# Optimization experiments

Hardware: AMD Instinct MI355X
Metric: run time of the kernel (lower is better)

The kernel has to match this reference:

```python
import jax, jax.numpy as jnp
import numpy as np

N, DEG, F_IN, H = 50000, 16, 128, 32
E = N * DEG


def _linear_params(key, out_f, in_f):
    kw, kb = jax.random.split(key)
    s = 1.0 / np.sqrt(in_f)
    W = jax.random.uniform(kw, (out_f, in_f), jnp.float32, -s, s)
    b = jax.random.uniform(kb, (out_f,), jnp.float32, -s, s)
    return W, b


def setup_inputs() -> dict:
    key = jax.random.key(0)
    ks = jax.random.split(key, 12)
    X = jax.random.normal(ks[0], (N, F_IN), jnp.float32)
    # DEG distinct nonzero offsets shared by all rows -> unique (src,dst) pairs,
    # so the COO tensor is already coalesced (no duplicate indices).
    offsets = jax.random.permutation(ks[1], jnp.arange(1, N))[:DEG]
    src = jnp.repeat(jnp.arange(N, dtype=jnp.int32), DEG)
    dst = ((src.reshape(N, DEG) + offsets[None, :].astype(jnp.int32)) % N).reshape(-1)
    D = jax.ops.segment_sum(jnp.ones((E,), jnp.float32), src, num_segments=N)
    wn1p, bn1p = _linear_params(ks[2], H, F_IN)      # convN1.pass_map
    wn1s, bn1s = _linear_params(ks[3], H, F_IN)      # convN1.self_map
    we1p, be1p = _linear_params(ks[4], H, 2 * H)     # convE1.pass_map
    we1s, be1s = _linear_params(ks[5], H, F_IN)      # convE1.self_map
    wn2p, bn2p = _linear_params(ks[6], H, H)         # convN2.pass_map
    wn2s, bn2s = _linear_params(ks[7], H, H)         # convN2.self_map
    we2p, be2p = _linear_params(ks[8], H, 2 * H)     # convE2.pass_map
    we2s, be2s = _linear_params(ks[9], H, H)         # convE2.self_map
    wc, bc = _linear_params(ks[10], 1, H)            # classifier
    return dict(X=X, src=src, dst=dst, D=D,
                wn1p=wn1p, bn1p=bn1p, wn1s=wn1s, bn1s=bn1s,
                we1p=we1p, be1p=be1p, we1s=we1s, be1s=be1s,
                wn2p=wn2p, bn2p=bn2p, wn2s=wn2s, bn2s=bn2s,
                we2p=we2p, be2p=be2p, we2s=we2s, be2s=be2s,
                wc=wc, bc=bc)


def reference(X, src, dst, D,
              wn1p, bn1p, wn1s, bn1s,
              we1p, be1p, we1s, be1s,
              wn2p, bn2p, wn2s, bn2s,
              we2p, be2p, we2s, be2s,
              wc, bc):
    n = X.shape[0]

    def node_conv(vals, Xn, wp, bp, ws, bs):
        # torch.sparse.sum(A, dim=1): sum edge values per source row
        Asum = jax.ops.segment_sum(vals, src, num_segments=n)
        return jax.nn.relu((Asum / D[:, None]) @ wp.T + bp + Xn @ ws.T + bs)

    def edge_conv(vals, Xn, wp, bp, ws, bs):
        X1, X2 = Xn[src], Xn[dst]
        Ef = jnp.concatenate([(X1 - X2) * 0.5, (X1 + X2) * 0.5], axis=-1)
        return jax.nn.relu(Ef @ wp.T + bp + vals @ ws.T + bs)

    # add_graph: edge features = |X[src] - X[dst]|
    vals0 = jnp.abs(X[src] - X[dst])            # (E, F_IN)
    X0 = jnp.zeros_like(X)                       # forward zeros node features
    Xn1 = node_conv(vals0, X0, wn1p, bn1p, wn1s, bn1s)   # (N, 32)
    vals1 = edge_conv(vals0, Xn1, we1p, be1p, we1s, be1s)  # (E, 32)
    Xn2 = node_conv(vals1, Xn1, wn2p, bn2p, wn2s, bn2s)  # (N, 32)
    vals2 = edge_conv(vals1, Xn2, we2p, be2p, we2s, be2s)  # (E, 32)
    SX = jax.nn.sigmoid(vals2 @ wc.T + bc)[:, 0]          # (E,)
    return SX
```

## Files before the change

### kernel.cpp

```cpp
#include <hip/hip_runtime.h>

#define DEG 16
#define F_IN 128
#define H 32

typedef __attribute__((ext_vector_type(8))) _Float16 f16x8;
typedef __attribute__((ext_vector_type(4))) float f32x4;
typedef __attribute__((ext_vector_type(4))) int i32x4;

union HS  { _Float16 f; unsigned short s; };
union HF4 { _Float16 h[4]; uint2 u; };

__device__ __forceinline__ float relu_f(float x) { return fmaxf(x, 0.0f); }

__device__ __forceinline__ f16x8 habs8(f16x8 a) {
    union { f16x8 h; i32x4 i; } u; u.h = a;
#pragma unroll
    for (int k = 0; k < 4; ++k) u.i[k] &= 0x7FFF7FFF;
    return u.h;
}

__global__ __launch_bounds__(256) void k_xhalf(
    const float* __restrict__ X, _Float16* __restrict__ Xh, long n8)
{
    const long t = (long)blockIdx.x * 256 + threadIdx.x;
    if (t >= n8) return;
    const float4* p = (const float4*)X + t * 2;
    const float4 a = p[0], b = p[1];
    f16x8 h;
    h[0] = (_Float16)a.x; h[1] = (_Float16)a.y; h[2] = (_Float16)a.z; h[3] = (_Float16)a.w;
    h[4] = (_Float16)b.x; h[5] = (_Float16)b.y; h[6] = (_Float16)b.z; h[7] = (_Float16)b.w;
    *(f16x8*)(Xh + t * 8) = h;
}

__global__ __launch_bounds__(256) void k_prep(
    const float* __restrict__ we1s, const float* __restrict__ we1p,
    const float* __restrict__ be1p, const float* __restrict__ be1s,
    const float* __restrict__ we2p, const float* __restrict__ we2s,
    const float* __restrict__ be2p, const float* __restrict__ be2s,
    const float* __restrict__ wn1p, const float* __restrict__ bn1p,
    const float* __restrict__ bn1s,
    const float* __restrict__ wn2p, const float* __restrict__ bn2p,
    const float* __restrict__ wn2s, const float* __restrict__ bn2s,
    _Float16* __restrict__ Wcat1, _Float16* __restrict__ Wcat2,
    _Float16* __restrict__ Wn1ph,
    _Float16* __restrict__ Wn2ph, _Float16* __restrict__ Wn2sh,
    float* __restrict__ bias1, float* __restrict__ bias2,
    float* __restrict__ biasn1, float* __restrict__ biasn2)
{
    const int t0 = blockIdx.x * 256 + threadIdx.x;
    const int stride = gridDim.x * 256;
    for (int idx = t0; idx < 32 * 192; idx += stride) {
        const int n = idx / 192, k = idx - n * 192;
        float w;
        if (k < 128)       w = we1s[n * 128 + k];
        else if (k < 160)  w = 0.5f * we1p[n * 64 + (k - 128)];
        else               w = 0.5f * we1p[n * 64 + 32 + (k - 160)];
        Wcat1[idx] = (_Float16)w;
    }
    for (int idx = t0; idx < 32 * 96; idx += stride) {
        const int n = idx / 96, k = idx - n * 96;
        float w;
        if (k < 32)       w = 0.5f * we2p[n * 64 + k];
        else if (k < 64)  w = 0.5f * we2p[n * 64 + 32 + (k - 32)];
        else              w = we2s[n * 32 + (k - 64)];
        Wcat2[idx] = (_Float16)w;
    }
    for (int idx = t0; idx < 32 * 128; idx += stride)
        Wn1ph[idx] = (_Float16)wn1p[idx];
    for (int idx = t0; idx < 32 * 32; idx += stride) {
        Wn2ph[idx] = (_Float16)wn2p[idx];
        Wn2sh[idx] = (_Float16)wn2s[idx];
    }
    if (t0 < H) {
        bias1[t0]  = be1p[t0] + be1s[t0];
        bias2[t0]  = be2p[t0] + be2s[t0];
        biasn1[t0] = bn1p[t0] + bn1s[t0];
        biasn2[t0] = bn2p[t0] + bn2s[t0];
    }
}

__global__ __launch_bounds__(64, 3) void k_p1(
    const _Float16* __restrict__ Xh, const int* __restrict__ dst,
    const float* __restrict__ D,
    const _Float16* __restrict__ Wcat1, const _Float16* __restrict__ Wn1ph,
    const float* __restrict__ biasn1,
    _Float16* __restrict__ t1h, _Float16* __restrict__ Xn1h, int N)
{
    const int lane = threadIdx.x;
    const int m = lane & 15, g = lane >> 4;
    const int i0 = blockIdx.x * 16;
    const int srow = (i0 + m < N) ? (i0 + m) : (N - 1);

    i32x4 dj4[4];
    {
        const i32x4* dp = (const i32x4*)(dst + (size_t)srow * DEG);
#pragma unroll
        for (int q = 0; q < 4; ++q) dj4[q] = dp[q];
    }
    f16x8 sv[4];
#pragma unroll
    for (int kb = 0; kb < 4; ++kb)
        sv[kb] = *(const f16x8*)(Xh + (size_t)srow * F_IN + kb * 32 + g * 8);
    f16x8 Bs[4][2], Bn[4][2];
#pragma unroll
    for (int kb = 0; kb < 4; ++kb)
#pragma unroll
        for (int t = 0; t < 2; ++t) {
            Bs[kb][t] = *(const f16x8*)(Wcat1 + (t * 16 + m) * 192 + kb * 32 + g * 8);
            Bn[kb][t] = *(const f16x8*)(Wn1ph + (t * 16 + m) * 128 + kb * 32 + g * 8);
        }

    f16x8 tvc[4], tvn[4];
#pragma unroll
    for (int kb = 0; kb < 4; ++kb)
        tvc[kb] = *(const f16x8*)(Xh + (size_t)dj4[0][0] * F_IN + kb * 32 + g * 8);

    f32x4 cn0 = {0.f,0.f,0.f,0.f}, cn1 = {0.f,0.f,0.f,0.f};
#pragma unroll
    for (int j = 0; j < 16; ++j) {
        if (j < 15) {
            const int dn = dj4[(j + 1) >> 2][(j + 1) & 3];
#pragma unroll
            for (int kb = 0; kb < 4; ++kb)
                tvn[kb] = *(const f16x8*)(Xh + (size_t)dn * F_IN + kb * 32 + g * 8);
        }
        f32x4 cs0 = {0.f,0.f,0.f,0.f}, cs1 = {0.f,0.f,0.f,0.f};
#pragma unroll
        for (int kb = 0; kb < 4; ++kb) {
            const f16x8 a = habs8(sv[kb] - tvc[kb]);
            cs0 = __builtin_amdgcn_mfma_f32_16x16x32_f16(a, Bs[kb][0], cs0, 0, 0, 0);
            cs1 = __builtin_amdgcn_mfma_f32_16x16x32_f16(a, Bs[kb][1], cs1, 0, 0, 0);
            cn0 = __builtin_amdgcn_mfma_f32_16x16x32_f16(a, Bn[kb][0], cn0, 0, 0, 0);
            cn1 = __builtin_amdgcn_mfma_f32_16x16x32_f16(a, Bn[kb][1], cn1, 0, 0, 0);
        }
        const size_t tb = ((size_t)blockIdx.x * 16 + j) * 512;
        HF4 a;
#pragma unroll
        for (int r = 0; r < 4; ++r) a.h[r] = (_Float16)cs0[r];
        *(uint2*)(t1h + tb + lane * 4) = a.u;
#pragma unroll
        for (int r = 0; r < 4; ++r) a.h[r] = (_Float16)cs1[r];
        *(uint2*)(t1h + tb + 256 + lane * 4) = a.u;
#pragma unroll
        for (int kb = 0; kb < 4; ++kb) tvc[kb] = tvn[kb];
    }
    const float bn0 = biasn1[m], bn1v = biasn1[16 + m];
#pragma unroll
    for (int r = 0; r < 4; ++r) {
        const int node = i0 + g * 4 + r;
        if (node < N) {
            const float invD = 1.0f / D[node];
            Xn1h[(size_t)node * H + m]      = (_Float16)relu_f(cn0[r] * invD + bn0);
            Xn1h[(size_t)node * H + 16 + m] = (_Float16)relu_f(cn1[r] * invD + bn1v);
        }
    }
}

__global__ __launch_bounds__(64, 4) void k_p2(
    const int* __restrict__ dst, const _Float16* __restrict__ Xn1h,
    const _Float16* __restrict__ Wcat1, const float* __restrict__ bias1,
    const _Float16* __restrict__ Wn2ph, const _Float16* __restrict__ Wn2sh,
    const float* __restrict__ biasn2, const float* __restrict__ D,
    _Float16* t1v1,
    _Float16* __restrict__ Xn2h, int N)
{
    __shared__ unsigned short RP[16 * 40];
    const int lane = threadIdx.x;
    const int m = lane & 15, g = lane >> 4;
    const int i0 = blockIdx.x * 16;
    const int srow = (i0 + m < N) ? (i0 + m) : (N - 1);

    i32x4 dj4[4];
    {
        const i32x4* dp = (const i32x4*)(dst + (size_t)srow * DEG);
#pragma unroll
        for (int q = 0; q < 4; ++q) dj4[q] = dp[q];
    }
    const f16x8 x1 = *(const f16x8*)(Xn1h + (size_t)srow * H + g * 8);
    f16x8 Bf[2][2];
#pragma unroll
    for (int kb = 0; kb < 2; ++kb)
#pragma unroll
        for (int t = 0; t < 2; ++t)
            Bf[kb][t] = *(const f16x8*)(Wcat1 + (t * 16 + m) * 192 + (4 + kb) * 32 + g * 8);

    f16x8 x2c, x2n;
    uint2 u0c, u1c, u0n, u1n;
    {
        const int d0 = dj4[0][0];
        x2c = *(const f16x8*)(Xn1h + (size_t)d0 * H + g * 8);
        const size_t tb = ((size_t)blockIdx.x * 16) * 512;
        u0c = *(const uint2*)(t1v1 + tb + lane * 4);
        u1c = *(const uint2*)(t1v1 + tb + 256 + lane * 4);
    }
    const float b0 = bias1[m], b1v = bias1[16 + m];
    f32x4 sB0 = {0.f,0.f,0.f,0.f}, sB1 = {0.f,0.f,0.f,0.f};
    const int rr = lane >> 2, qq = lane & 3;
#pragma unroll
    for (int j = 0; j < 16; ++j) {
        if (j < 15) {
            const int dn = dj4[(j + 1) >> 2][(j + 1) & 3];
            x2n = *(const f16x8*)(Xn1h + (size_t)dn * H + g * 8);
            const size_t tbn = ((size_t)blockIdx.x * 16 + j + 1) * 512;
            u0n = *(const uint2*)(t1v1 + tbn + lane * 4);
            u1n = *(const uint2*)(t1v1 + tbn + 256 + lane * 4);
        }
        f32x4 c0, c1;
        { HF4 a; a.u = u0c;
#pragma unroll
          for (int r = 0; r < 4; ++r) c0[r] = (float)a.h[r];
          a.u = u1c;
#pragma unroll
          for (int r = 0; r < 4; ++r) c1[r] = (float)a.h[r]; }
        const f16x8 ad = x1 - x2c;
        const f16x8 aS = x1 + x2c;
        c0 = __builtin_amdgcn_mfma_f32_16x16x32_f16(ad, Bf[0][0], c0, 0, 0, 0);
        c1 = __builtin_amdgcn_mfma_f32_16x16x32_f16(ad, Bf[0][1], c1, 0, 0, 0);
        c0 = __builtin_amdgcn_mfma_f32_16x16x32_f16(aS, Bf[1][0], c0, 0, 0, 0);
        c1 = __builtin_amdgcn_mfma_f32_16x16x32_f16(aS, Bf[1][1], c1, 0, 0, 0);
#pragma unroll
        for (int r = 0; r < 4; ++r) {
            const float v0 = relu_f(c0[r] + b0);
            const float v1 = relu_f(c1[r] + b1v);
            HS h0, h1; h0.f = (_Float16)v0; h1.f = (_Float16)v1;
            RP[(g * 4 + r) * 40 + m]      = h0.s;
            RP[(g * 4 + r) * 40 + 16 + m] = h1.s;
            sB0[r] += v0; sB1[r] += v1;
        }
        const size_t tb = ((size_t)blockIdx.x * 16 + j) * 512;
        const i32x4 v = *(const i32x4*)(RP + rr * 40 + qq * 8);
        *(i32x4*)(t1v1 + tb + rr * 32 + qq * 8) = v;
        x2c = x2n; u0c = u0n; u1c = u1n;
    }
    _Float16* RPh = (_Float16*)RP;
#pragma unroll
    for (int r = 0; r < 4; ++r) {
        const int node = i0 + g * 4 + r;
        const float invD = 1.0f / D[(node < N) ? node : (N - 1)];
        RPh[(g * 4 + r) * 40 + m]      = (_Float16)(sB0[r] * invD);
        RPh[(g * 4 + r) * 40 + 16 + m] = (_Float16)(sB1[r] * invD);
    }
    const f16x8 aF = *(const f16x8*)(RPh + m * 40 + g * 8);
    f16x8 Bp[2], Bs2[2];
#pragma unroll
    for (int t = 0; t < 2; ++t) {
        Bp[t]  = *(const f16x8*)(Wn2ph + (t * 16 + m) * H + g * 8);
        Bs2[t] = *(const f16x8*)(Wn2sh + (t * 16 + m) * H + g * 8);
    }
    f32x4 c0 = {0.f,0.f,0.f,0.f}, c1 = {0.f,0.f,0.f,0.f};
    c0 = __builtin_amdgcn_mfma_f32_16x16x32_f16(aF, Bp[0], c0, 0, 0, 0);
    c1 = __builtin_amdgcn_mfma_f32_16x16x32_f16(aF, Bp[1], c1, 0, 0, 0);
    c0 = __builtin_amdgcn_mfma_f32_16x16x32_f16(x1, Bs2[0], c0, 0, 0, 0);
    c1 = __builtin_amdgcn_mfma_f32_16x16x32_f16(x1, Bs2[1], c1, 0, 0, 0);
    const float bp0 = biasn2[m], bp1 = biasn2[16 + m];
#pragma unroll
    for (int r = 0; r < 4; ++r) {
        const int node = i0 + g * 4 + r;
        if (node < N) {
            Xn2h[(size_t)node * H + m]      = (_Float16)relu_f(c0[r] + bp0);
            Xn2h[(size_t)node * H + 16 + m] = (_Float16)relu_f(c1[r] + bp1);
        }
    }
}

__global__ __launch_bounds__(64, 4) void k_p3(
    const _Float16* __restrict__ Xn2h, const int* __restrict__ dst,
    const _Float16* __restrict__ vals1,
    const _Float16* __restrict__ Wcat2, const float* __restrict__ bias2,
    const float* __restrict__ wc, const float* __restrict__ bc,
    float* __restrict__ out, int N)
{
    __shared__ float outS[16 * 16];
    const int lane = threadIdx.x;
    const int m = lane & 15, g = lane >> 4;
    const int i0 = blockIdx.x * 16;
    const int srow = (i0 + m < N) ? (i0 + m) : (N - 1);

    i32x4 dj4[4];
    {
        const i32x4* dp = (const i32x4*)(dst + (size_t)srow * DEG);
#pragma unroll
        for (int q = 0; q < 4; ++q) dj4[q] = dp[q];
    }
    const f16x8 x1 = *(const f16x8*)(Xn2h + (size_t)srow * H + g * 8);
    f16x8 Bf[3][2];
#pragma unroll
    for (int kb = 0; kb < 3; ++kb)
#pragma unroll
        for (int t = 0; t < 2; ++t)
            Bf[kb][t] = *(const f16x8*)(Wcat2 + (t * 16 + m) * 96 + kb * 32 + g * 8);

    f16x8 x2b[2], avb[2];
#pragma unroll
    for (int s = 0; s < 2; ++s) {
        const int dn = dj4[s >> 2][s & 3];
        x2b[s] = *(const f16x8*)(Xn2h + (size_t)dn * H + g * 8);
        avb[s] = *(const f16x8*)(vals1 + ((size_t)blockIdx.x * 16 + s) * 512 + m * 32 + g * 8);
    }
    const float b0 = bias2[m], b1v = bias2[16 + m];
    const float w0 = wc[m], w1 = wc[16 + m];
#pragma unroll
    for (int j = 0; j < 16; ++j) {
        const int s = j & 1;
        const f16x8 x2 = x2b[s];
        const f16x8 av = avb[s];
        if (j < 14) {
            const int dn = dj4[(j + 2) >> 2][(j + 2) & 3];
            x2b[s] = *(const f16x8*)(Xn2h + (size_t)dn * H + g * 8);
            avb[s] = *(const f16x8*)(vals1 + ((size_t)blockIdx.x * 16 + j + 2) * 512 + m * 32 + g * 8);
        }
        const f16x8 ad = x1 - x2;
        const f16x8 aS = x1 + x2;
        f32x4 c0 = {0.f,0.f,0.f,0.f}, c1 = {0.f,0.f,0.f,0.f};
        c0 = __builtin_amdgcn_mfma_f32_16x16x32_f16(ad, Bf[0][0], c0, 0, 0, 0);
        c1 = __builtin_amdgcn_mfma_f32_16x16x32_f16(ad, Bf[0][1], c1, 0, 0, 0);
        c0 = __builtin_amdgcn_mfma_f32_16x16x32_f16(aS, Bf[1][0], c0, 0, 0, 0);
        c1 = __builtin_amdgcn_mfma_f32_16x16x32_f16(aS, Bf[1][1], c1, 0, 0, 0);
        c0 = __builtin_amdgcn_mfma_f32_16x16x32_f16(av, Bf[2][0], c0, 0, 0, 0);
        c1 = __builtin_amdgcn_mfma_f32_16x16x32_f16(av, Bf[2][1], c1, 0, 0, 0);

        float sr[4];
#pragma unroll
        for (int r = 0; r < 4; ++r)
            sr[r] = relu_f(c0[r] + b0) * w0 + relu_f(c1[r] + b1v) * w1;
#pragma unroll
        for (int mask = 1; mask < 16; mask <<= 1) {
#pragma unroll
            for (int r = 0; r < 4; ++r)
                sr[r] += __shfl_xor(sr[r], mask);
        }
        if (m == 0) {
#pragma unroll
            for (int r = 0; r < 4; ++r)
                outS[(g * 4 + r) * 16 + j] = sr[r];
        }
    }
    {
        const float bcv = bc[0];
        const float* s = outS + lane * 4;
        float4 o;
        o.x = 1.0f / (1.0f + __expf(-(s[0] + bcv)));
        o.y = 1.0f / (1.0f + __expf(-(s[1] + bcv)));
        o.z = 1.0f / (1.0f + __expf(-(s[2] + bcv)));
        o.w = 1.0f / (1.0f + __expf(-(s[3] + bcv)));
        if (i0 + 16 <= N || (i0 + (lane >> 2)) < N)
            *(float4*)(out + (size_t)i0 * DEG + lane * 4) = o;
    }
}

extern "C" void kernel_launch(void* const* d_in, const int* in_sizes, int n_in,
                              void* d_out, int out_size, void* d_ws, size_t ws_size,
                              hipStream_t stream)
{
    const float* X    = (const float*)d_in[0];
    const int*   dst  = (const int*)  d_in[2];
    const float* D    = (const float*)d_in[3];
    const float* wn1p = (const float*)d_in[4];
    const float* bn1p = (const float*)d_in[5];
    const float* bn1s = (const float*)d_in[7];
    const float* we1p = (const float*)d_in[8];
    const float* be1p = (const float*)d_in[9];
    const float* we1s = (const float*)d_in[10];
    const float* be1s = (const float*)d_in[11];
    const float* wn2p = (const float*)d_in[12];
    const float* bn2p = (const float*)d_in[13];
    const float* wn2s = (const float*)d_in[14];
    const float* bn2s = (const float*)d_in[15];
    const float* we2p = (const float*)d_in[16];
    const float* be2p = (const float*)d_in[17];
    const float* we2s = (const float*)d_in[18];
    const float* be2s = (const float*)d_in[19];
    const float* wc   = (const float*)d_in[20];
    const float* bc   = (const float*)d_in[21];

    const int N = in_sizes[3];
    const int nbW = (N + 15) / 16;
    const size_t Epad = (size_t)nbW * 16 * DEG;

    char* w = (char*)d_ws;
    _Float16* t1v1  = (_Float16*)w;  w += Epad * H * 2;
    _Float16* Xh    = (_Float16*)w;  w += (size_t)N * F_IN * 2;
    _Float16* Xn1h  = (_Float16*)w;  w += (size_t)N * H * 2;
    _Float16* Xn2h  = (_Float16*)w;  w += (size_t)N * H * 2;
    _Float16* Wcat1 = (_Float16*)w;  w += 32 * 192 * 2;
    _Float16* Wcat2 = (_Float16*)w;  w += 32 * 96 * 2;
    _Float16* Wn1ph = (_Float16*)w;  w += 32 * 128 * 2;
    _Float16* Wn2ph = (_Float16*)w;  w += 32 * 32 * 2;
    _Float16* Wn2sh = (_Float16*)w;  w += 32 * 32 * 2;
    float* bias1  = (float*)w;       w += H * 4;
    float* bias2  = (float*)w;       w += H * 4;
    float* biasn1 = (float*)w;       w += H * 4;
    float* biasn2 = (float*)w;       w += H * 4;
    float* outp = (float*)d_out;

    const long n8 = (long)N * F_IN / 8;
    const int nbX = (int)((n8 + 255) / 256);

    k_xhalf<<<nbX, 256, 0, stream>>>(X, Xh, n8);
    k_prep<<<32, 256, 0, stream>>>(we1s, we1p, be1p, be1s, we2p, we2s, be2p, be2s,
                                   wn1p, bn1p, bn1s, wn2p, bn2p, wn2s, bn2s,
                                   Wcat1, Wcat2, Wn1ph, Wn2ph, Wn2sh,
                                   bias1, bias2, biasn1, biasn2);
    k_p1<<<nbW, 64, 0, stream>>>(Xh, dst, D, Wcat1, Wn1ph, biasn1, t1v1, Xn1h, N);
    k_p2<<<nbW, 64, 0, stream>>>(dst, Xn1h, Wcat1, bias1, Wn2ph, Wn2sh,
                                 biasn2, D, t1v1, Xn2h, N);
    k_p3<<<nbW, 64, 0, stream>>>(Xn2h, dst, t1v1, Wcat2, bias2, wc, bc, outp, N);
}
```

Baseline: 199.7 us.

## Pack four waves per block and deepen gather prefetch to two edges

Each kernel now runs four independent 16-node chunks per 256-thread block instead of one wave per block, with per-wave shared-memory slices and early exit for out-of-range chunks. k_p1 and k_p2 switch from single-edge to two-edge-ahead double-buffered prefetch of the gathered neighbour rows. k_p1's MFMA loop is written out by hand. The aim is lower block-launch and scheduling overhead from tiny 64-thread blocks, plus more latency hiding for the random gathers. In exchange, register pressure rises under the new launch bounds, which could lower occupancy or cause spills.

```diff
diff --git a/kernel.cpp b/kernel.cpp
--- a/kernel.cpp
+++ b/kernel.cpp
@@ -80,16 +80,19 @@
     }
 }
 
-__global__ __launch_bounds__(64, 3) void k_p1(
+__global__ __launch_bounds__(256, 4) void k_p1(
     const _Float16* __restrict__ Xh, const int* __restrict__ dst,
     const float* __restrict__ D,
     const _Float16* __restrict__ Wcat1, const _Float16* __restrict__ Wn1ph,
     const float* __restrict__ biasn1,
     _Float16* __restrict__ t1h, _Float16* __restrict__ Xn1h, int N)
 {
-    const int lane = threadIdx.x;
+    const int wave = threadIdx.x >> 6;
+    const int lane = threadIdx.x & 63;
+    const int chunk = blockIdx.x * 4 + wave;
+    const int i0 = chunk * 16;
+    if (i0 >= N) return;
     const int m = lane & 15, g = lane >> 4;
-    const int i0 = blockIdx.x * 16;
     const int srow = (i0 + m < N) ? (i0 + m) : (N - 1);
 
     i32x4 dj4[4];
@@ -111,30 +114,46 @@
             Bn[kb][t] = *(const f16x8*)(Wn1ph + (t * 16 + m) * 128 + kb * 32 + g * 8);
         }
 
-    f16x8 tvc[4], tvn[4];
-#pragma unroll
-    for (int kb = 0; kb < 4; ++kb)
-        tvc[kb] = *(const f16x8*)(Xh + (size_t)dj4[0][0] * F_IN + kb * 32 + g * 8);
+    f16x8 tv[2][4];
+#pragma unroll
+    for (int s = 0; s < 2; ++s) {
+        const int dn = dj4[s >> 2][s & 3];
+#pragma unroll
+        for (int kb = 0; kb < 4; ++kb)
+            tv[s][kb] = *(const f16x8*)(Xh + (size_t)dn * F_IN + kb * 32 + g * 8);
+    }
 
     f32x4 cn0 = {0.f,0.f,0.f,0.f}, cn1 = {0.f,0.f,0.f,0.f};
 #pragma unroll
     for (int j = 0; j < 16; ++j) {
-        if (j < 15) {
-            const int dn = dj4[(j + 1) >> 2][(j + 1) & 3];
+        const int s = j & 1;
+        f16x8 a0 = tv[s][0], a1 = tv[s][1], a2 = tv[s][2], a3 = tv[s][3];
+        if (j < 14) {
+            const int dn = dj4[(j + 2) >> 2][(j + 2) & 3];
 #pragma unroll
             for (int kb = 0; kb < 4; ++kb)
-                tvn[kb] = *(const f16x8*)(Xh + (size_t)dn * F_IN + kb * 32 + g * 8);
-        }
+                tv[s][kb] = *(const f16x8*)(Xh + (size_t)dn * F_IN + kb * 32 + g * 8);
+        }
+        a0 = habs8(sv[0] - a0); a1 = habs8(sv[1] - a1);
+        a2 = habs8(sv[2] - a2); a3 = habs8(sv[3] - a3);
         f32x4 cs0 = {0.f,0.f,0.f,0.f}, cs1 = {0.f,0.f,0.f,0.f};
-#pragma unroll
-        for (int kb = 0; kb < 4; ++kb) {
-            const f16x8 a = habs8(sv[kb] - tvc[kb]);
-            cs0 = __builtin_amdgcn_mfma_f32_16x16x32_f16(a, Bs[kb][0], cs0, 0, 0, 0);
-            cs1 = __builtin_amdgcn_mfma_f32_16x16x32_f16(a, Bs[kb][1], cs1, 0, 0, 0);
-            cn0 = __builtin_amdgcn_mfma_f32_16x16x32_f16(a, Bn[kb][0], cn0, 0, 0, 0);
-            cn1 = __builtin_amdgcn_mfma_f32_16x16x32_f16(a, Bn[kb][1], cn1, 0, 0, 0);
-        }
-        const size_t tb = ((size_t)blockIdx.x * 16 + j) * 512;
+        cs0 = __builtin_amdgcn_mfma_f32_16x16x32_f16(a0, Bs[0][0], cs0, 0, 0, 0);
+        cs1 = __builtin_amdgcn_mfma_f32_16x16x32_f16(a0, Bs[0][1], cs1, 0, 0, 0);
+        cn0 = __builtin_amdgcn_mfma_f32_16x16x32_f16(a0, Bn[0][0], cn0, 0, 0, 0);
+        cn1 = __builtin_amdgcn_mfma_f32_16x16x32_f16(a0, Bn[0][1], cn1, 0, 0, 0);
+        cs0 = __builtin_amdgcn_mfma_f32_16x16x32_f16(a1, Bs[1][0], cs0, 0, 0, 0);
+        cs1 = __builtin_amdgcn_mfma_f32_16x16x32_f16(a1, Bs[1][1], cs1, 0, 0, 0);
+        cn0 = __builtin_amdgcn_mfma_f32_16x16x32_f16(a1, Bn[1][0], cn0, 0, 0, 0);
+        cn1 = __builtin_amdgcn_mfma_f32_16x16x32_f16(a1, Bn[1][1], cn1, 0, 0, 0);
+        cs0 = __builtin_amdgcn_mfma_f32_16x16x32_f16(a2, Bs[2][0], cs0, 0, 0, 0);
+        cs1 = __builtin_amdgcn_mfma_f32_16x16x32_f16(a2, Bs[2][1], cs1, 0, 0, 0);
+        cn0 = __builtin_amdgcn_mfma_f32_16x16x32_f16(a2, Bn[2][0], cn0, 0, 0, 0);
+        cn1 = __builtin_amdgcn_mfma_f32_16x16x32_f16(a2, Bn[2][1], cn1, 0, 0, 0);
+        cs0 = __builtin_amdgcn_mfma_f32_16x16x32_f16(a3, Bs[3][0], cs0, 0, 0, 0);
+        cs1 = __builtin_amdgcn_mfma_f32_16x16x32_f16(a3, Bs[3][1], cs1, 0, 0, 0);
+        cn0 = __builtin_amdgcn_mfma_f32_16x16x32_f16(a3, Bn[3][0], cn0, 0, 0, 0);
+        cn1 = __builtin_amdgcn_mfma_f32_16x16x32_f16(a3, Bn[3][1], cn1, 0, 0, 0);
+        const size_t tb = ((size_t)chunk * 16 + j) * 512;
         HF4 a;
 #pragma unroll
         for (int r = 0; r < 4; ++r) a.h[r] = (_Float16)cs0[r];
@@ -142,8 +161,6 @@
 #pragma unroll
         for (int r = 0; r < 4; ++r) a.h[r] = (_Float16)cs1[r];
         *(uint2*)(t1h + tb + 256 + lane * 4) = a.u;
-#pragma unroll
-        for (int kb = 0; kb < 4; ++kb) tvc[kb] = tvn[kb];
     }
     const float bn0 = biasn1[m], bn1v = biasn1[16 + m];
 #pragma unroll
@@ -157,7 +174,7 @@
     }
 }
 
-__global__ __launch_bounds__(64, 4) void k_p2(
+__global__ __launch_bounds__(256, 4) void k_p2(
     const int* __restrict__ dst, const _Float16* __restrict__ Xn1h,
     const _Float16* __restrict__ Wcat1, const float* __restrict__ bias1,
     const _Float16* __restrict__ Wn2ph, const _Float16* __restrict__ Wn2sh,
@@ -165,10 +182,14 @@
     _Float16* t1v1,
     _Float16* __restrict__ Xn2h, int N)
 {
-    __shared__ unsigned short RP[16 * 40];
-    const int lane = threadIdx.x;
+    __shared__ unsigned short RPall[4][16 * 40];
+    const int wave = threadIdx.x >> 6;
+    const int lane = threadIdx.x & 63;
+    const int chunk = blockIdx.x * 4 + wave;
+    const int i0 = chunk * 16;
+    if (i0 >= N) return;
+    unsigned short* RP = RPall[wave];
     const int m = lane & 15, g = lane >> 4;
-    const int i0 = blockIdx.x * 16;
     const int srow = (i0 + m < N) ? (i0 + m) : (N - 1);
 
     i32x4 dj4[4];
@@ -185,36 +206,40 @@
         for (int t = 0; t < 2; ++t)
             Bf[kb][t] = *(const f16x8*)(Wcat1 + (t * 16 + m) * 192 + (4 + kb) * 32 + g * 8);
 
-    f16x8 x2c, x2n;
-    uint2 u0c, u1c, u0n, u1n;
-    {
-        const int d0 = dj4[0][0];
-        x2c = *(const f16x8*)(Xn1h + (size_t)d0 * H + g * 8);
-        const size_t tb = ((size_t)blockIdx.x * 16) * 512;
-        u0c = *(const uint2*)(t1v1 + tb + lane * 4);
-        u1c = *(const uint2*)(t1v1 + tb + 256 + lane * 4);
+    f16x8 x2b[2];
+    uint2 u0b[2], u1b[2];
+#pragma unroll
+    for (int s = 0; s < 2; ++s) {
+        const int dn = dj4[s >> 2][s & 3];
+        x2b[s] = *(const f16x8*)(Xn1h + (size_t)dn * H + g * 8);
+        const size_t tb = ((size_t)chunk * 16 + s) * 512;
+        u0b[s] = *(const uint2*)(t1v1 + tb + lane * 4);
+        u1b[s] = *(const uint2*)(t1v1 + tb + 256 + lane * 4);
     }
     const float b0 = bias1[m], b1v = bias1[16 + m];
     f32x4 sB0 = {0.f,0.f,0.f,0.f}, sB1 = {0.f,0.f,0.f,0.f};
     const int rr = lane >> 2, qq = lane & 3;
 #pragma unroll
     for (int j = 0; j < 16; ++j) {
-        if (j < 15) {
-            const int dn = dj4[(j + 1) >> 2][(j + 1) & 3];
-            x2n = *(const f16x8*)(Xn1h + (size_t)dn * H + g * 8);
-            const size_t tbn = ((size_t)blockIdx.x * 16 + j + 1) * 512;
-            u0n = *(const uint2*)(t1v1 + tbn + lane * 4);
-            u1n = *(const uint2*)(t1v1 + tbn + 256 + lane * 4);
+        const int s = j & 1;
+        const f16x8 x2 = x2b[s];
+        const uint2 u0 = u0b[s], u1 = u1b[s];
+        if (j < 14) {
+            const int dn = dj4[(j + 2) >> 2][(j + 2) & 3];
+            x2b[s] = *(const f16x8*)(Xn1h + (size_t)dn * H + g * 8);
+            const size_t tbn = ((size_t)chunk * 16 + j + 2) * 512;
+            u0b[s] = *(const uint2*)(t1v1 + tbn + lane * 4);
+            u1b[s] = *(const uint2*)(t1v1 + tbn + 256 + lane * 4);
         }
         f32x4 c0, c1;
-        { HF4 a; a.u = u0c;
+        { HF4 a; a.u = u0;
 #pragma unroll
           for (int r = 0; r < 4; ++r) c0[r] = (float)a.h[r];
-          a.u = u1c;
+          a.u = u1;
 #pragma unroll
           for (int r = 0; r < 4; ++r) c1[r] = (float)a.h[r]; }
-        const f16x8 ad = x1 - x2c;
-        const f16x8 aS = x1 + x2c;
+        const f16x8 ad = x1 - x2;
+        const f16x8 aS = x1 + x2;
         c0 = __builtin_amdgcn_mfma_f32_16x16x32_f16(ad, Bf[0][0], c0, 0, 0, 0);
         c1 = __builtin_amdgcn_mfma_f32_16x16x32_f16(ad, Bf[0][1], c1, 0, 0, 0);
         c0 = __builtin_amdgcn_mfma_f32_16x16x32_f16(aS, Bf[1][0], c0, 0, 0, 0);
@@ -228,10 +253,9 @@
             RP[(g * 4 + r) * 40 + 16 + m] = h1.s;
             sB0[r] += v0; sB1[r] += v1;
         }
-        const size_t tb = ((size_t)blockIdx.x * 16 + j) * 512;
+        const size_t tb = ((size_t)chunk * 16 + j) * 512;
         const i32x4 v = *(const i32x4*)(RP + rr * 40 + qq * 8);
         *(i32x4*)(t1v1 + tb + rr * 32 + qq * 8) = v;
-        x2c = x2n; u0c = u0n; u1c = u1n;
     }
     _Float16* RPh = (_Float16*)RP;
 #pragma unroll
@@ -264,17 +288,21 @@
     }
 }
 
-__global__ __launch_bounds__(64, 4) void k_p3(
+__global__ __launch_bounds__(256, 4) void k_p3(
     const _Float16* __restrict__ Xn2h, const int* __restrict__ dst,
     const _Float16* __restrict__ vals1,
     const _Float16* __restrict__ Wcat2, const float* __restrict__ bias2,
     const float* __restrict__ wc, const float* __restrict__ bc,
     float* __restrict__ out, int N)
 {
-    __shared__ float outS[16 * 16];
-    const int lane = threadIdx.x;
+    __shared__ float outSall[4][16 * 16];
+    const int wave = threadIdx.x >> 6;
+    const int lane = threadIdx.x & 63;
+    const int chunk = blockIdx.x * 4 + wave;
+    const int i0 = chunk * 16;
+    if (i0 >= N) return;
+    float* outS = outSall[wave];
     const int m = lane & 15, g = lane >> 4;
-    const int i0 = blockIdx.x * 16;
     const int srow = (i0 + m < N) ? (i0 + m) : (N - 1);
 
     i32x4 dj4[4];
@@ -296,7 +324,7 @@
     for (int s = 0; s < 2; ++s) {
         const int dn = dj4[s >> 2][s & 3];
         x2b[s] = *(const f16x8*)(Xn2h + (size_t)dn * H + g * 8);
-        avb[s] = *(const f16x8*)(vals1 + ((size_t)blockIdx.x * 16 + s) * 512 + m * 32 + g * 8);
+        avb[s] = *(const f16x8*)(vals1 + ((size_t)chunk * 16 + s) * 512 + m * 32 + g * 8);
     }
     const float b0 = bias2[m], b1v = bias2[16 + m];
     const float w0 = wc[m], w1 = wc[16 + m];
@@ -308,7 +336,7 @@
         if (j < 14) {
             const int dn = dj4[(j + 2) >> 2][(j + 2) & 3];
             x2b[s] = *(const f16x8*)(Xn2h + (size_t)dn * H + g * 8);
-            avb[s] = *(const f16x8*)(vals1 + ((size_t)blockIdx.x * 16 + j + 2) * 512 + m * 32 + g * 8);
+            avb[s] = *(const f16x8*)(vals1 + ((size_t)chunk * 16 + j + 2) * 512 + m * 32 + g * 8);
         }
         const f16x8 ad = x1 - x2;
         const f16x8 aS = x1 + x2;
@@ -376,6 +404,7 @@
 
     const int N = in_sizes[3];
     const int nbW = (N + 15) / 16;
+    const int nbB = (nbW + 3) / 4;
     const size_t Epad = (size_t)nbW * 16 * DEG;
 
     char* w = (char*)d_ws;
@@ -402,8 +431,8 @@
                                    wn1p, bn1p, bn1s, wn2p, bn2p, wn2s, bn2s,
                                    Wcat1, Wcat2, Wn1ph, Wn2ph, Wn2sh,
                                    bias1, bias2, biasn1, biasn2);
-    k_p1<<<nbW, 64, 0, stream>>>(Xh, dst, D, Wcat1, Wn1ph, biasn1, t1v1, Xn1h, N);
-    k_p2<<<nbW, 64, 0, stream>>>(dst, Xn1h, Wcat1, bias1, Wn2ph, Wn2sh,
-                                 biasn2, D, t1v1, Xn2h, N);
-    k_p3<<<nbW, 64, 0, stream>>>(Xn2h, dst, t1v1, Wcat2, bias2, wc, bc, outp, N);
-}
+    k_p1<<<nbB, 256, 0, stream>>>(Xh, dst, D, Wcat1, Wn1ph, biasn1, t1v1, Xn1h, N);
+    k_p2<<<nbB, 256, 0, stream>>>(dst, Xn1h, Wcat1, bias1, Wn2ph, Wn2sh,
+                                  biasn2, D, t1v1, Xn2h, N);
+    k_p3<<<nbB, 256, 0, stream>>>(Xn2h, dst, t1v1, Wcat2, bias2, wc, bc, outp, N);
+}
```

Result: slower. 292.4 us (+46.4%).
